# Optimization experiments

Hardware: AMD Instinct MI355X
Metric: run time of the kernel (lower is better)

## Reference

```python
import jax, jax.numpy as jnp
import numpy as np

NEG_INF = jnp.finfo(jnp.float32).min


def setup_inputs() -> dict:
    key = jax.random.key(0)
    ks = jax.random.split(key, 5)
    B, S, D = 2, 2048, 1024
    std = 0.02
    return {
        "x": jax.random.normal(ks[0], (B, S, D), dtype=jnp.float32),
        "attention_mask": jnp.ones((B, S), dtype=jnp.int32),
        "Wq": jax.random.normal(ks[1], (D, D), dtype=jnp.float32) * std,
        "Wk": jax.random.normal(ks[2], (D, D), dtype=jnp.float32) * std,
        "Wv": jax.random.normal(ks[3], (D, D), dtype=jnp.float32) * std,
        "Wo": jax.random.normal(ks[4], (D, D), dtype=jnp.float32) * std,
    }


def reference(x, attention_mask, Wq, Wk, Wv, Wo):
    B, S, D = x.shape
    H = 16
    Hd = D // H
    scale = jnp.float32(np.sqrt(Hd))

    # F.linear uses W @ x^T, i.e. x @ W.T
    def proj(x, W):
        return jnp.einsum('bsd,ed->bse', x, W).reshape(B, S, H, Hd).transpose(0, 2, 1, 3)

    q = proj(x, Wq)  # [B,H,S,Hd]
    k = proj(x, Wk)
    v = proj(x, Wv)

    scores = jnp.einsum('bhqd,bhkd->bhqk', q, k) / scale  # [B,H,S,S]
    causal = jnp.triu(jnp.ones((S, S), dtype=bool), k=1)
    scores = jnp.where(causal[None, None, :, :], NEG_INF, scores)
    key_pad = (attention_mask == 0)[:, None, None, :]  # [B,1,1,S]
    scores = jnp.where(key_pad, NEG_INF, scores)

    attn = jax.nn.softmax(scores, axis=-1)
    out = jnp.einsum('bhqk,bhkd->bhqd', attn, v)  # [B,H,S,Hd]
    out = out.transpose(0, 2, 1, 3).reshape(B, S, D)
    return jnp.einsum('bsd,ed->bse', out, Wo)
```

## Files before the change

### kernel.cpp

```cpp
#include <hip/hip_runtime.h>
#include <hip/hip_bf16.h>

typedef __attribute__((ext_vector_type(8))) short bf16x8;
typedef __attribute__((ext_vector_type(4))) short bf16x4;
typedef __attribute__((ext_vector_type(4))) float f32x4;

#define LOG2E 1.4426950408889634f
#define NEGF  -3.0e38f

__device__ __forceinline__ void gl_lds16(const void* g, void* l) {
  __builtin_amdgcn_global_load_lds((const __attribute__((address_space(1))) void*)g,
                                   (__attribute__((address_space(3))) void*)l, 16, 0, 0);
}

__device__ __forceinline__ ushort f2bu(float x) {
  __hip_bfloat16 h = __float2bfloat16(x);
  return *(ushort*)&h;
}

__global__ __launch_bounds__(256) void cast_bf16_k(const float* __restrict__ in,
                                                   ushort* __restrict__ out, int n4) {
  int i = blockIdx.x * 256 + threadIdx.x;
  if (i >= n4) return;
  float4 f = ((const float4*)in)[i];
  ushort4 u;
  u.x = f2bu(f.x); u.y = f2bu(f.y); u.z = f2bu(f.z); u.w = f2bu(f.w);
  ((ushort4*)out)[i] = u;
}

__global__ __launch_bounds__(256) void cast_w4_k(const float* __restrict__ a, const float* __restrict__ b,
                                                 const float* __restrict__ c, const float* __restrict__ d,
                                                 ushort* __restrict__ oa, ushort* __restrict__ ob,
                                                 ushort* __restrict__ oc, ushort* __restrict__ od) {
  int i = blockIdx.x * 256 + threadIdx.x;
  int wsel = i >> 18, j = i & 262143;
  const float* src = wsel == 0 ? a : wsel == 1 ? b : wsel == 2 ? c : d;
  ushort* dst      = wsel == 0 ? oa : wsel == 1 ? ob : wsel == 2 ? oc : od;
  float4 f = ((const float4*)src)[j];
  ushort4 u;
  u.x = f2bu(f.x); u.y = f2bu(f.y); u.z = f2bu(f.z); u.w = f2bu(f.w);
  ((ushort4*)dst)[j] = u;
}

template<int OUT_BF16>
__device__ __forceinline__ void gemm_body(const ushort* __restrict__ A, const ushort* __restrict__ B,
                                          void* __restrict__ C, int M, int N, int Kd, float scale,
                                          int bm, int bn, ushort (*As)[4096], ushort (*Bs)[4096]) {
  const int t  = threadIdx.x;
  const int l  = t & 63;
  const int w  = t >> 6;
  const int lr = l & 15, lg = l >> 4;
  const int wr = (w >> 1) * 64, wc = (w & 1) * 64;

  auto stage = [&](int buf, int ktE) {
    int idx = t, row = idx >> 2, ch = idx & 3;
    gl_lds16(A + (size_t)(bm + row) * Kd + ktE + ch * 8, &As[buf][idx * 8]);
    gl_lds16(B + (size_t)(bn + row) * Kd + ktE + ch * 8, &Bs[buf][idx * 8]);
    idx = t + 256; row = idx >> 2; ch = idx & 3;
    gl_lds16(A + (size_t)(bm + row) * Kd + ktE + ch * 8, &As[buf][idx * 8]);
    gl_lds16(B + (size_t)(bn + row) * Kd + ktE + ch * 8, &Bs[buf][idx * 8]);
  };

  f32x4 acc[4][4] = {};
  const int nK = Kd >> 5;

  stage(0, 0);
  stage(1, 32);
  int cur = 0;
  for (int k5 = 0; k5 < nK; ++k5) {
    if (k5 + 2 < nK) {
      int nb = cur + 2; if (nb >= 3) nb -= 3;
      stage(nb, (k5 + 2) << 5);
      asm volatile("s_waitcnt vmcnt(8)" ::: "memory");
    } else if (k5 + 1 < nK) {
      asm volatile("s_waitcnt vmcnt(4)" ::: "memory");
    } else {
      asm volatile("s_waitcnt vmcnt(0)" ::: "memory");
    }
    __builtin_amdgcn_s_barrier();

    bf16x8 af[4], bfr[4];
#pragma unroll
    for (int m = 0; m < 4; ++m)
      af[m] = *(const bf16x8*)&As[cur][(wr + m * 16 + lr) * 32 + lg * 8];
#pragma unroll
    for (int n = 0; n < 4; ++n)
      bfr[n] = *(const bf16x8*)&Bs[cur][(wc + n * 16 + lr) * 32 + lg * 8];
#pragma unroll
    for (int m = 0; m < 4; ++m)
#pragma unroll
      for (int n = 0; n < 4; ++n)
        acc[m][n] = __builtin_amdgcn_mfma_f32_16x16x32_bf16(af[m], bfr[n], acc[m][n], 0, 0, 0);

    __builtin_amdgcn_s_barrier();
    ++cur; if (cur >= 3) cur -= 3;
  }

#pragma unroll
  for (int m = 0; m < 4; ++m)
#pragma unroll
    for (int n = 0; n < 4; ++n)
#pragma unroll
      for (int j = 0; j < 4; ++j) {
        int row = bm + wr + m * 16 + lg * 4 + j;
        int col = bn + wc + n * 16 + lr;
        float v = acc[m][n][j] * scale;
        if (OUT_BF16) {
          ((ushort*)C)[(size_t)row * N + col] = f2bu(v);
        } else {
          ((float*)C)[(size_t)row * N + col] = v;
        }
      }
}

__global__ __launch_bounds__(256)
void gemm_qkv(const ushort* __restrict__ A, const ushort* __restrict__ Wq, const ushort* __restrict__ Wk,
              const ushort* __restrict__ Wv, ushort* __restrict__ Qo, ushort* __restrict__ Ko,
              ushort* __restrict__ Vo, int M, int Kd) {
  __shared__ __attribute__((aligned(16))) ushort As[3][4096];
  __shared__ __attribute__((aligned(16))) ushort Bs[3][4096];
  int by = blockIdx.y;
  int which = by >> 3;
  const ushort* B = which == 0 ? Wq : which == 1 ? Wk : Wv;
  ushort* C       = which == 0 ? Qo : which == 1 ? Ko : Vo;
  float scale = which == 0 ? 0.125f : 1.0f;
  gemm_body<1>(A, B, C, M, 1024, Kd, scale, blockIdx.x * 128, (by & 7) * 128, As, Bs);
}

__global__ __launch_bounds__(256)
void gemm_out64(const ushort* __restrict__ A, const ushort* __restrict__ B, float* __restrict__ C,
                int M, int N, int Kd) {
  __shared__ __attribute__((aligned(16))) ushort As[3][2048];
  __shared__ __attribute__((aligned(16))) ushort Bs[3][4096];
  const int t  = threadIdx.x;
  const int l  = t & 63;
  const int w  = t >> 6;
  const int lr = l & 15, lg = l >> 4;
  const int wr = (w >> 1) * 32, wc = (w & 1) * 64;
  const int bm = blockIdx.x * 64, bn = blockIdx.y * 128;

  auto stage = [&](int buf, int ktE) {
    int idx = t, row = idx >> 2, ch = idx & 3;
    gl_lds16(A + (size_t)(bm + row) * Kd + ktE + ch * 8, &As[buf][idx * 8]);
    row = idx >> 2; ch = idx & 3;
    gl_lds16(B + (size_t)(bn + row) * Kd + ktE + ch * 8, &Bs[buf][idx * 8]);
    idx = t + 256; row = idx >> 2; ch = idx & 3;
    gl_lds16(B + (size_t)(bn + row) * Kd + ktE + ch * 8, &Bs[buf][idx * 8]);
  };

  f32x4 acc[2][4] = {};
  const int nK = Kd >> 5;

  stage(0, 0);
  stage(1, 32);
  int cur = 0;
  for (int k5 = 0; k5 < nK; ++k5) {
    if (k5 + 2 < nK) {
      int nb = cur + 2; if (nb >= 3) nb -= 3;
      stage(nb, (k5 + 2) << 5);
      asm volatile("s_waitcnt vmcnt(6)" ::: "memory");
    } else if (k5 + 1 < nK) {
      asm volatile("s_waitcnt vmcnt(3)" ::: "memory");
    } else {
      asm volatile("s_waitcnt vmcnt(0)" ::: "memory");
    }
    __builtin_amdgcn_s_barrier();

    bf16x8 af[2], bfr[4];
#pragma unroll
    for (int m = 0; m < 2; ++m)
      af[m] = *(const bf16x8*)&As[cur][(wr + m * 16 + lr) * 32 + lg * 8];
#pragma unroll
    for (int n = 0; n < 4; ++n)
      bfr[n] = *(const bf16x8*)&Bs[cur][(wc + n * 16 + lr) * 32 + lg * 8];
#pragma unroll
    for (int m = 0; m < 2; ++m)
#pragma unroll
      for (int n = 0; n < 4; ++n)
        acc[m][n] = __builtin_amdgcn_mfma_f32_16x16x32_bf16(af[m], bfr[n], acc[m][n], 0, 0, 0);

    __builtin_amdgcn_s_barrier();
    ++cur; if (cur >= 3) cur -= 3;
  }

#pragma unroll
  for (int m = 0; m < 2; ++m)
#pragma unroll
    for (int n = 0; n < 4; ++n)
#pragma unroll
      for (int j = 0; j < 4; ++j) {
        int row = bm + wr + m * 16 + lg * 4 + j;
        int col = bn + wc + n * 16 + lr;
        C[(size_t)row * N + col] = acc[m][n][j];
      }
}

__device__ __forceinline__ void online_sm(f32x4 s4[4], float& m_, float& l_, f32x4 o[4],
                                          int lg, bf16x8& pa0_out, bf16x8& pa1_out) {
  float tm = NEGF;
#pragma unroll
  for (int c = 0; c < 4; ++c)
#pragma unroll
    for (int j = 0; j < 4; ++j) tm = fmaxf(tm, s4[c][j]);
  tm = fmaxf(tm, __shfl_xor(tm, 16));
  tm = fmaxf(tm, __shfl_xor(tm, 32));

  bool need = !__all(tm - m_ <= 8.0f);
  float mn = need ? fmaxf(m_, tm) : m_;
  float scl = mn * LOG2E;
  if (need) {
    float alpha = exp2f(m_ * LOG2E - scl);
    m_ = mn;
    l_ *= alpha;
    float a0 = __shfl(alpha, lg * 4 + 0, 16);
    float a1 = __shfl(alpha, lg * 4 + 1, 16);
    float a2 = __shfl(alpha, lg * 4 + 2, 16);
    float a3 = __shfl(alpha, lg * 4 + 3, 16);
#pragma unroll
    for (int dt = 0; dt < 4; ++dt) {
      o[dt][0] *= a0; o[dt][1] *= a1; o[dt][2] *= a2; o[dt][3] *= a3;
    }
  }

  float rs = 0.f;
#pragma unroll
  for (int c = 0; c < 4; ++c)
#pragma unroll
    for (int j = 0; j < 4; ++j) {
      float p = exp2f(s4[c][j] * LOG2E - scl);
      rs += p;
      s4[c][j] = p;
    }
  rs += __shfl_xor(rs, 16);
  rs += __shfl_xor(rs, 32);
  l_ += rs;

  union { bf16x8 v; ushort u[8]; } pa0, pa1;
#pragma unroll
  for (int j = 0; j < 4; ++j) {
    pa0.u[j]     = f2bu(s4[0][j]);
    pa0.u[4 + j] = f2bu(s4[1][j]);
    pa1.u[j]     = f2bu(s4[2][j]);
    pa1.u[4 + j] = f2bu(s4[3][j]);
  }
  pa0_out = pa0.v;
  pa1_out = pa1.v;
}

__global__ __launch_bounds__(512, 4)
void attn_k(const ushort* __restrict__ Q, const ushort* __restrict__ K,
            const ushort* __restrict__ V, const int* __restrict__ mask,
            ushort* __restrict__ O) {
  const int S = 2048, D = 1024;
  __shared__ __attribute__((aligned(16))) ushort Ks[4][4096];
  __shared__ __attribute__((aligned(16))) ushort Vs[4][4096];
  __shared__ unsigned long long Msb[32];

  const int t = threadIdx.x;
  const int l = t & 63, w = t >> 6;
  const int lr = l & 15, lg = l >> 4;

  int f = blockIdx.x;
  int pp = (f >> 3) & 15;
  int ss = ((f >> 8) & 1) ? 15 - pp : pp;
  int bh = (f & 7) | (((f >> 7) & 3) << 3);
  int h = bh & 15, b = bh >> 4;
  const int nt = 2 * ss + 2;
  const int q0 = ss * 128;
  const int ktd = 2 * ss + (w >> 2);
  const int cdi = w & 3;
  const size_t bS = (size_t)b * S;

  const ushort* qptr = Q + (bS + q0 + w * 16 + lr) * D + h * 64;
  bf16x8 qf0 = *(const bf16x8*)(qptr + lg * 8);
  bf16x8 qf1 = *(const bf16x8*)(qptr + 32 + lg * 8);

  const ushort* Kbh = K + bS * D + h * 64;
  const ushort* Vbh = V + bS * D + h * 64;
  const int* mbase = mask + bS;

  for (int kk = w; kk < nt; kk += 8) {
    unsigned long long mb = __ballot(mbase[kk * 64 + l] != 0);
    if (l == 0) Msb[kk] = mb;
  }
  asm volatile("s_waitcnt lgkmcnt(0)" ::: "memory");
  __builtin_amdgcn_sched_barrier(0);

  float m_ = -INFINITY, l_ = 0.f;
  f32x4 o[4] = {};

  auto stage = [&](int buf, int kt) {
    { int idx = t; int row = idx >> 3, ch = idx & 7;
      gl_lds16(Kbh + (size_t)(kt * 64 + row) * D + ((ch ^ (row & 7)) * 8), &Ks[buf][idx * 8]); }
    { int idx = t; int dg = idx >> 7, kq = (idx >> 3) & 15, jj = (idx >> 1) & 3, hf = idx & 1;
      gl_lds16(Vbh + (size_t)(kt * 64 + kq * 4 + jj) * D + dg * 16 + hf * 8, &Vs[buf][idx * 8]); }
  };

  stage(0, 0);
  stage(1, 1);

  for (int kt = 0; kt < nt; ++kt) {
    const int cur = kt & 3;
    if (kt + 2 < nt) {
      stage((kt + 2) & 3, kt + 2);
      asm volatile("s_waitcnt vmcnt(4)" ::: "memory");
    } else if (kt + 1 < nt) {
      asm volatile("s_waitcnt vmcnt(2)" ::: "memory");
    } else {
      asm volatile("s_waitcnt vmcnt(0)" ::: "memory");
    }
    __builtin_amdgcn_s_barrier();

    if (kt <= ktd) {
      unsigned long long mb = Msb[kt];
      const bool diag = (kt == ktd);
      const int cmax = diag ? cdi : 3;

      f32x4 s4[4];
      __builtin_amdgcn_s_setprio(1);
#pragma unroll
      for (int c = 0; c < 4; ++c) {
        if (c <= cmax) {
          int row = c * 16 + lr;
          bf16x8 kf0 = *(const bf16x8*)&Ks[cur][row * 64 + ((lg ^ (row & 7)) << 3)];
          bf16x8 kf1 = *(const bf16x8*)&Ks[cur][row * 64 + (((4 + lg) ^ (row & 7)) << 3)];
          f32x4 sc = {0.f, 0.f, 0.f, 0.f};
          sc = __builtin_amdgcn_mfma_f32_16x16x32_bf16(kf0, qf0, sc, 0, 0, 0);
          sc = __builtin_amdgcn_mfma_f32_16x16x32_bf16(kf1, qf1, sc, 0, 0, 0);
          if (diag && c == cmax) {
            int qg = cdi * 16 + lr, kb = c * 16 + lg * 4;
#pragma unroll
            for (int j = 0; j < 4; ++j)
              if (kb + j > qg) sc[j] = NEGF;
          }
          s4[c] = sc;
        } else {
          s4[c] = (f32x4){NEGF, NEGF, NEGF, NEGF};
        }
      }
      __builtin_amdgcn_s_setprio(0);

      if (~mb != 0ull) {
#pragma unroll
        for (int c = 0; c < 4; ++c)
#pragma unroll
          for (int j = 0; j < 4; ++j)
            if (!((mb >> (c * 16 + lg * 4 + j)) & 1)) s4[c][j] = NEGF;
      }

      bf16x8 pa0, pa1;
      online_sm(s4, m_, l_, o, lg, pa0, pa1);

      __builtin_amdgcn_s_setprio(1);
#pragma unroll
      for (int dt = 0; dt < 4; ++dt) {
        const __attribute__((address_space(3))) ushort* vp =
            (const __attribute__((address_space(3))) ushort*)&Vs[cur][0] + dt * 1024 + lg * 64 + lr * 4;
        bf16x4 h0, h1, h2, h3;
        asm volatile(
            "ds_read_b64_tr_b16 %0, %4\n\t"
            "ds_read_b64_tr_b16 %1, %4 offset:512\n\t"
            "ds_read_b64_tr_b16 %2, %4 offset:1024\n\t"
            "ds_read_b64_tr_b16 %3, %4 offset:1536\n\t"
            "s_waitcnt lgkmcnt(0)"
            : "=&v"(h0), "=&v"(h1), "=&v"(h2), "=&v"(h3)
            : "v"(vp));
        bf16x8 vb0 = __builtin_shufflevector(h0, h1, 0, 1, 2, 3, 4, 5, 6, 7);
        bf16x8 vb1 = __builtin_shufflevector(h2, h3, 0, 1, 2, 3, 4, 5, 6, 7);
        o[dt] = __builtin_amdgcn_mfma_f32_16x16x32_bf16(pa0, vb0, o[dt], 0, 0, 0);
        o[dt] = __builtin_amdgcn_mfma_f32_16x16x32_bf16(pa1, vb1, o[dt], 0, 0, 0);
      }
      __builtin_amdgcn_s_setprio(0);
    }
  }

  float inv = 1.0f / l_;
  float v0 = __shfl(inv, lg * 4 + 0, 16);
  float v1 = __shfl(inv, lg * 4 + 1, 16);
  float v2 = __shfl(inv, lg * 4 + 2, 16);
  float v3 = __shfl(inv, lg * 4 + 3, 16);
#pragma unroll
  for (int dt = 0; dt < 4; ++dt) {
    size_t col = (size_t)h * 64 + dt * 16 + lr;
    size_t r0 = bS + q0 + w * 16 + lg * 4;
    O[(r0 + 0) * D + col] = f2bu(o[dt][0] * v0);
    O[(r0 + 1) * D + col] = f2bu(o[dt][1] * v1);
    O[(r0 + 2) * D + col] = f2bu(o[dt][2] * v2);
    O[(r0 + 3) * D + col] = f2bu(o[dt][3] * v3);
  }
}

extern "C" void kernel_launch(void* const* d_in, const int* in_sizes, int n_in,
                              void* d_out, int out_size, void* d_ws, size_t ws_size,
                              hipStream_t stream) {
  const float* x    = (const float*)d_in[0];
  const int*   mask = (const int*)d_in[1];
  const float* Wq   = (const float*)d_in[2];
  const float* Wk   = (const float*)d_in[3];
  const float* Wv   = (const float*)d_in[4];
  const float* Wo   = (const float*)d_in[5];
  float* out = (float*)d_out;

  const int B = 2, S = 2048, D = 1024;
  const int M = B * S;

  char* ws = (char*)d_ws;
  ushort* xb  = (ushort*)(ws);
  ushort* wqb = (ushort*)(ws + (8ull  << 20));
  ushort* wkb = (ushort*)(ws + (10ull << 20));
  ushort* wvb = (ushort*)(ws + (12ull << 20));
  ushort* wob = (ushort*)(ws + (14ull << 20));
  ushort* Qb  = (ushort*)(ws + (16ull << 20));
  ushort* Kb  = (ushort*)(ws + (24ull << 20));
  ushort* Vb  = (ushort*)(ws + (32ull << 20));
  ushort* AO  = (ushort*)(ws + (40ull << 20));

  int nx4 = M * D / 4;
  cast_bf16_k<<<(nx4 + 255) / 256, 256, 0, stream>>>(x, xb, nx4);
  cast_w4_k<<<4096, 256, 0, stream>>>(Wq, Wk, Wv, Wo, wqb, wkb, wvb, wob);

  dim3 gq(M / 128, 24);
  gemm_qkv<<<gq, 256, 0, stream>>>(xb, wqb, wkb, wvb, Qb, Kb, Vb, M, D);

  attn_k<<<512, 512, 0, stream>>>(Qb, Kb, Vb, mask, AO);

  dim3 go(M / 64, D / 128);
  gemm_out64<<<go, 256, 0, stream>>>(AO, wob, out, M, D, D);
}
```

Before: 119.5 us.

## Process key tiles in pairs with two independent online-softmax streams per wave

The attention loop now handles two 64-key tiles per iteration, keeping separate running max, sum and output accumulators for the even and odd tiles, and merges them at the end. Staging loads two tiles at once and adds a second barrier per pair, which halves the number of barrier and wait points and gives the scheduler independent MFMA chains to interleave. LDS offsets are also precomputed once. The cost is roughly doubled accumulator registers, which can lower occupancy, plus a final merge step.

```diff
diff --git a/kernel.cpp b/kernel.cpp
--- a/kernel.cpp
+++ b/kernel.cpp
@@ -266,8 +266,10 @@
   int bh = (f & 7) | (((f >> 7) & 3) << 3);
   int h = bh & 15, b = bh >> 4;
   const int nt = 2 * ss + 2;
+  const int np = ss + 1;
   const int q0 = ss * 128;
-  const int ktd = 2 * ss + (w >> 2);
+  const bool hiW = (w >> 2);
+  const int npO = hiW ? np : np - 1;
   const int cdi = w & 3;
   const size_t bS = (size_t)b * S;
 
@@ -279,6 +281,17 @@
   const ushort* Vbh = V + bS * D + h * 64;
   const int* mbase = mask + bS;
 
+  int koffA[4], koffB[4];
+#pragma unroll
+  for (int c = 0; c < 4; ++c) {
+    int row = c * 16 + lr;
+    koffA[c] = row * 64 + ((lg ^ (row & 7)) << 3);
+    koffB[c] = row * 64 + (((4 + lg) ^ (row & 7)) << 3);
+  }
+  int voff[4];
+#pragma unroll
+  for (int dt = 0; dt < 4; ++dt) voff[dt] = dt * 1024 + lg * 64 + lr * 4;
+
   for (int kk = w; kk < nt; kk += 8) {
     unsigned long long mb = __ballot(mbase[kk * 64 + l] != 0);
     if (l == 0) Msb[kk] = mb;
@@ -286,76 +299,126 @@
   asm volatile("s_waitcnt lgkmcnt(0)" ::: "memory");
   __builtin_amdgcn_sched_barrier(0);
 
-  float m_ = -INFINITY, l_ = 0.f;
-  f32x4 o[4] = {};
-
-  auto stage = [&](int buf, int kt) {
+  float mE = -INFINITY, lE = 0.f, mO = -INFINITY, lO = 0.f;
+  f32x4 oE[4] = {}, oO[4] = {};
+
+  auto stage = [&](int p) {
+    int s0 = (p & 1) << 1;
+    int k0 = 2 * p, k1 = 2 * p + 1;
     { int idx = t; int row = idx >> 3, ch = idx & 7;
-      gl_lds16(Kbh + (size_t)(kt * 64 + row) * D + ((ch ^ (row & 7)) * 8), &Ks[buf][idx * 8]); }
+      size_t go = (size_t)row * D + ((ch ^ (row & 7)) * 8);
+      gl_lds16(Kbh + (size_t)(k0 * 64) * D + go, &Ks[s0][idx * 8]);
+      gl_lds16(Kbh + (size_t)(k1 * 64) * D + go, &Ks[s0 + 1][idx * 8]); }
     { int idx = t; int dg = idx >> 7, kq = (idx >> 3) & 15, jj = (idx >> 1) & 3, hf = idx & 1;
-      gl_lds16(Vbh + (size_t)(kt * 64 + kq * 4 + jj) * D + dg * 16 + hf * 8, &Vs[buf][idx * 8]); }
+      size_t go = (size_t)(kq * 4 + jj) * D + dg * 16 + hf * 8;
+      gl_lds16(Vbh + (size_t)(k0 * 64) * D + go, &Vs[s0][idx * 8]);
+      gl_lds16(Vbh + (size_t)(k1 * 64) * D + go, &Vs[s0 + 1][idx * 8]); }
   };
 
-  stage(0, 0);
-  stage(1, 1);
-
-  for (int kt = 0; kt < nt; ++kt) {
-    const int cur = kt & 3;
-    if (kt + 2 < nt) {
-      stage((kt + 2) & 3, kt + 2);
-      asm volatile("s_waitcnt vmcnt(4)" ::: "memory");
-    } else if (kt + 1 < nt) {
-      asm volatile("s_waitcnt vmcnt(2)" ::: "memory");
-    } else {
-      asm volatile("s_waitcnt vmcnt(0)" ::: "memory");
-    }
-    __builtin_amdgcn_s_barrier();
-
-    if (kt <= ktd) {
-      unsigned long long mb = Msb[kt];
-      const bool diag = (kt == ktd);
-      const int cmax = diag ? cdi : 3;
-
-      f32x4 s4[4];
-      __builtin_amdgcn_s_setprio(1);
-#pragma unroll
-      for (int c = 0; c < 4; ++c) {
-        if (c <= cmax) {
-          int row = c * 16 + lr;
-          bf16x8 kf0 = *(const bf16x8*)&Ks[cur][row * 64 + ((lg ^ (row & 7)) << 3)];
-          bf16x8 kf1 = *(const bf16x8*)&Ks[cur][row * 64 + (((4 + lg) ^ (row & 7)) << 3)];
+  stage(0);
+  if (np > 1) stage(1);
+
+  for (int p = 0; p < np; ++p) {
+    const int s0 = (p & 1) << 1;
+    if (p + 1 < np) asm volatile("s_waitcnt vmcnt(4)" ::: "memory");
+    else            asm volatile("s_waitcnt vmcnt(0)" ::: "memory");
+    __builtin_amdgcn_s_barrier();
+
+    const bool actO  = (p < npO);
+    const bool diagE = (!hiW) && (p == ss);
+    const bool diagO = hiW && (p == ss);
+    const int cmaxE = diagE ? cdi : 3;
+    const int cmaxO = diagO ? cdi : 3;
+    unsigned long long mbE = Msb[2 * p];
+    unsigned long long mbO = Msb[2 * p + 1];
+
+    f32x4 sE[4], sO[4];
+    __builtin_amdgcn_s_setprio(1);
+#pragma unroll
+    for (int c = 0; c < 4; ++c) {
+      if (c <= cmaxE) {
+        bf16x8 kf0 = *(const bf16x8*)&Ks[s0][koffA[c]];
+        bf16x8 kf1 = *(const bf16x8*)&Ks[s0][koffB[c]];
+        f32x4 sc = {0.f, 0.f, 0.f, 0.f};
+        sc = __builtin_amdgcn_mfma_f32_16x16x32_bf16(kf0, qf0, sc, 0, 0, 0);
+        sc = __builtin_amdgcn_mfma_f32_16x16x32_bf16(kf1, qf1, sc, 0, 0, 0);
+        if (diagE && c == cmaxE) {
+          int qg = cdi * 16 + lr, kb = c * 16 + lg * 4;
+#pragma unroll
+          for (int j = 0; j < 4; ++j)
+            if (kb + j > qg) sc[j] = NEGF;
+        }
+        sE[c] = sc;
+      } else {
+        sE[c] = (f32x4){NEGF, NEGF, NEGF, NEGF};
+      }
+      if (actO) {
+        if (c <= cmaxO) {
+          bf16x8 kf0 = *(const bf16x8*)&Ks[s0 + 1][koffA[c]];
+          bf16x8 kf1 = *(const bf16x8*)&Ks[s0 + 1][koffB[c]];
           f32x4 sc = {0.f, 0.f, 0.f, 0.f};
           sc = __builtin_amdgcn_mfma_f32_16x16x32_bf16(kf0, qf0, sc, 0, 0, 0);
           sc = __builtin_amdgcn_mfma_f32_16x16x32_bf16(kf1, qf1, sc, 0, 0, 0);
-          if (diag && c == cmax) {
+          if (diagO && c == cmaxO) {
             int qg = cdi * 16 + lr, kb = c * 16 + lg * 4;
 #pragma unroll
             for (int j = 0; j < 4; ++j)
               if (kb + j > qg) sc[j] = NEGF;
           }
-          s4[c] = sc;
+          sO[c] = sc;
         } else {
-          s4[c] = (f32x4){NEGF, NEGF, NEGF, NEGF};
+          sO[c] = (f32x4){NEGF, NEGF, NEGF, NEGF};
         }
       }
-      __builtin_amdgcn_s_setprio(0);
-
-      if (~mb != 0ull) {
-#pragma unroll
-        for (int c = 0; c < 4; ++c)
-#pragma unroll
-          for (int j = 0; j < 4; ++j)
-            if (!((mb >> (c * 16 + lg * 4 + j)) & 1)) s4[c][j] = NEGF;
-      }
-
-      bf16x8 pa0, pa1;
-      online_sm(s4, m_, l_, o, lg, pa0, pa1);
-
+    }
+    __builtin_amdgcn_s_setprio(0);
+
+    if (~mbE != 0ull) {
+#pragma unroll
+      for (int c = 0; c < 4; ++c)
+#pragma unroll
+        for (int j = 0; j < 4; ++j)
+          if (!((mbE >> (c * 16 + lg * 4 + j)) & 1)) sE[c][j] = NEGF;
+    }
+    if (actO && (~mbO != 0ull)) {
+#pragma unroll
+      for (int c = 0; c < 4; ++c)
+#pragma unroll
+        for (int j = 0; j < 4; ++j)
+          if (!((mbO >> (c * 16 + lg * 4 + j)) & 1)) sO[c][j] = NEGF;
+    }
+
+    bf16x8 paE0, paE1;
+    online_sm(sE, mE, lE, oE, lg, paE0, paE1);
+    __builtin_amdgcn_s_setprio(1);
+#pragma unroll
+    for (int dt = 0; dt < 4; ++dt) {
+      const __attribute__((address_space(3))) ushort* vp =
+          (const __attribute__((address_space(3))) ushort*)&Vs[s0][0] + voff[dt];
+      bf16x4 h0, h1, h2, h3;
+      asm volatile(
+          "ds_read_b64_tr_b16 %0, %4\n\t"
+          "ds_read_b64_tr_b16 %1, %4 offset:512\n\t"
+          "ds_read_b64_tr_b16 %2, %4 offset:1024\n\t"
+          "ds_read_b64_tr_b16 %3, %4 offset:1536\n\t"
+          "s_waitcnt lgkmcnt(0)"
+          : "=&v"(h0), "=&v"(h1), "=&v"(h2), "=&v"(h3)
+          : "v"(vp));
+      bf16x8 vb0 = __builtin_shufflevector(h0, h1, 0, 1, 2, 3, 4, 5, 6, 7);
+      bf16x8 vb1 = __builtin_shufflevector(h2, h3, 0, 1, 2, 3, 4, 5, 6, 7);
+      oE[dt] = __builtin_amdgcn_mfma_f32_16x16x32_bf16(paE0, vb0, oE[dt], 0, 0, 0);
+      oE[dt] = __builtin_amdgcn_mfma_f32_16x16x32_bf16(paE1, vb1, oE[dt], 0, 0, 0);
+    }
+    __builtin_amdgcn_s_setprio(0);
+
+    if (actO) {
+      bf16x8 paO0, paO1;
+      online_sm(sO, mO, lO, oO, lg, paO0, paO1);
       __builtin_amdgcn_s_setprio(1);
 #pragma unroll
       for (int dt = 0; dt < 4; ++dt) {
         const __attribute__((address_space(3))) ushort* vp =
-            (const __attribute__((address_space(3))) ushort*)&Vs[cur][0] + dt * 1024 + lg * 64 + lr * 4;
+            (const __attribute__((address_space(3))) ushort*)&Vs[s0 + 1][0] + voff[dt];
         bf16x4 h0, h1, h2, h3;
         asm volatile(
             "ds_read_b64_tr_b16 %0, %4\n\t"
@@ -367,26 +430,32 @@
             : "v"(vp));
         bf16x8 vb0 = __builtin_shufflevector(h0, h1, 0, 1, 2, 3, 4, 5, 6, 7);
         bf16x8 vb1 = __builtin_shufflevector(h2, h3, 0, 1, 2, 3, 4, 5, 6, 7);
-        o[dt] = __builtin_amdgcn_mfma_f32_16x16x32_bf16(pa0, vb0, o[dt], 0, 0, 0);
-        o[dt] = __builtin_amdgcn_mfma_f32_16x16x32_bf16(pa1, vb1, o[dt], 0, 0, 0);
+        oO[dt] = __builtin_amdgcn_mfma_f32_16x16x32_bf16(paO0, vb0, oO[dt], 0, 0, 0);
+        oO[dt] = __builtin_amdgcn_mfma_f32_16x16x32_bf16(paO1, vb1, oO[dt], 0, 0, 0);
       }
       __builtin_amdgcn_s_setprio(0);
     }
-  }
-
+
+    __builtin_amdgcn_s_barrier();
+    if (p + 2 < np) stage(p + 2);
+  }
+
+  float m = fmaxf(mE, mO);
+  float aE = exp2f((mE - m) * LOG2E);
+  float aO = (mO == -INFINITY) ? 0.f : exp2f((mO - m) * LOG2E);
+  float l_ = lE * aE + lO * aO;
   float inv = 1.0f / l_;
-  float v0 = __shfl(inv, lg * 4 + 0, 16);
-  float v1 = __shfl(inv, lg * 4 + 1, 16);
-  float v2 = __shfl(inv, lg * 4 + 2, 16);
-  float v3 = __shfl(inv, lg * 4 + 3, 16);
+  float fE = aE * inv, fO = aO * inv;
 #pragma unroll
   for (int dt = 0; dt < 4; ++dt) {
     size_t col = (size_t)h * 64 + dt * 16 + lr;
     size_t r0 = bS + q0 + w * 16 + lg * 4;
-    O[(r0 + 0) * D + col] = f2bu(o[dt][0] * v0);
-    O[(r0 + 1) * D + col] = f2bu(o[dt][1] * v1);
-    O[(r0 + 2) * D + col] = f2bu(o[dt][2] * v2);
-    O[(r0 + 3) * D + col] = f2bu(o[dt][3] * v3);
+#pragma unroll
+    for (int j = 0; j < 4; ++j) {
+      float e = __shfl(fE, lg * 4 + j, 16);
+      float o2 = __shfl(fO, lg * 4 + j, 16);
+      O[(r0 + j) * D + col] = f2bu(oE[dt][j] * e + oO[dt][j] * o2);
+    }
   }
 }
 
```

After: 118.1 us. About the same (-1.2%).
